# Kernel optimization log

Hardware: AMD Instinct MI355X
Metric: run time of the kernel (lower is better)

The kernel has to match this reference:

```python
import jax, jax.numpy as jnp
import numpy as np

H = 512  # hidden_dimension
B = 32
S = 2048


def setup_inputs() -> dict:
    key = jax.random.key(0)
    k1, k2, k3, k4, k5, k6 = jax.random.split(key, 6)
    decoder_hide = jax.random.normal(k1, (B, H), dtype=jnp.float32)
    encoder_out = jax.random.normal(k2, (B, S, 2 * H), dtype=jnp.float32)
    mask = jax.random.randint(k3, (B, S), 0, 2, dtype=jnp.int32)
    bound = 1.0 / np.sqrt(3 * H)
    W_attn = jax.random.uniform(k4, (3 * H, H), minval=-bound, maxval=bound, dtype=jnp.float32)
    b_attn = jax.random.uniform(k5, (H,), minval=-bound, maxval=bound, dtype=jnp.float32)
    bound_v = 1.0 / np.sqrt(H)
    v_w = jax.random.uniform(k6, (H,), minval=-bound_v, maxval=bound_v, dtype=jnp.float32)
    return {"decoder_hide": decoder_hide, "encoder_out": encoder_out, "mask": mask,
            "W_attn": W_attn, "b_attn": b_attn, "v_w": v_w}


def reference(decoder_hide, encoder_out, mask, W_attn, b_attn, v_w):
    # Split the concat-linear: cat((h, enc)) @ W == h @ W[:H] + enc @ W[H:]
    W_h = W_attn[:H]        # [H, H]
    W_e = W_attn[H:]        # [2H, H]
    dec_proj = decoder_hide @ W_h + b_attn                 # [B, H]
    enc_proj = jnp.einsum('bse,eh->bsh', encoder_out, W_e)  # [B, S, H]
    energy = jnp.tanh(enc_proj + dec_proj[:, None, :])      # [B, S, H]
    attention = jnp.einsum('bsh,h->bs', energy, v_w)        # [B, S]
    attention = jnp.where(mask == 0, jnp.float32(-100000.0), attention)
    return jax.nn.softmax(attention, axis=1)
```

## Files before the change

### kernel.cpp

```cpp
#include <hip/hip_runtime.h>
#include <hip/hip_bf16.h>
#include <math.h>

#define Hdim 512
#define Bdim 32
#define Sdim 2048
#define Kdim 1024
#define Mtot (Bdim * Sdim)

#define BM 128
#define BK 64

typedef __attribute__((ext_vector_type(8))) short short8;
typedef __attribute__((ext_vector_type(4))) float floatx4;

__device__ __forceinline__ short f2bf(float f) {
    union { float f; unsigned u; } v; v.f = f;
    unsigned r = v.u + 0x7fffu + ((v.u >> 16) & 1u);
    return (short)(r >> 16);
}

__device__ __forceinline__ short8 cvt8(float4 a, float4 b) {
    union { short8 s; __hip_bfloat162 h[4]; } u;
    u.h[0] = __float22bfloat162_rn(make_float2(a.x, a.y));
    u.h[1] = __float22bfloat162_rn(make_float2(a.z, a.w));
    u.h[2] = __float22bfloat162_rn(make_float2(b.x, b.y));
    u.h[3] = __float22bfloat162_rn(make_float2(b.z, b.w));
    return u.s;
}

__device__ __forceinline__ float fast_tanh(float x) {
    float ax = fabsf(x);
    float e  = __expf(-2.0f * ax);
    float r  = (1.0f - e) * __builtin_amdgcn_rcpf(1.0f + e);
    return copysignf(r, x);
}

__global__ __launch_bounds__(256) void prep_kernel(
    const float* __restrict__ W_attn, const float* __restrict__ dec,
    const float* __restrict__ b_attn, short* __restrict__ Wbp,
    float* __restrict__ dec_proj)
{
    const int t = threadIdx.x;
    if (blockIdx.x < 512) {
        const float* We = W_attn + Hdim * Hdim;
        __shared__ short tile[32][33];
        const int k0 = (blockIdx.x >> 4) * 32;
        const int n0 = (blockIdx.x & 15) * 32;
        const int r = t >> 5, c = t & 31;
        #pragma unroll
        for (int rr = 0; rr < 4; ++rr)
            tile[r + rr * 8][c] = f2bf(We[(size_t)(k0 + r + rr * 8) * Hdim + n0 + c]);
        __syncthreads();
        if (t < 128) {
            const int n_loc = t >> 2;
            const int q     = t & 3;
            const int nt    = (n0 + n_loc) >> 4;
            const int lnn   = (n0 + n_loc) & 15;
            const int ks    = k0 >> 5;
            short8 v;
            #pragma unroll
            for (int r2 = 0; r2 < 8; ++r2) v[r2] = tile[q * 8 + r2][n_loc];
            ((short8*)Wbp)[((nt * 32 + ks) * 64) + q * 16 + lnn] = v;
        }
    } else {
        __shared__ float partl[2][128];
        const int bid = blockIdx.x - 512;
        const int b  = bid >> 2;
        const int cb = bid & 3;
        const int c  = cb * 128 + (t & 127);
        const int kh = t >> 7;
        float acc = 0.0f;
        const int kbeg = kh * 256, kend = kbeg + 256;
        #pragma unroll 8
        for (int k = kbeg; k < kend; ++k)
            acc = fmaf(dec[b * Hdim + k], W_attn[(size_t)k * Hdim + c], acc);
        partl[kh][t & 127] = acc;
        __syncthreads();
        if (t < 128)
            dec_proj[b * Hdim + cb * 128 + t] = partl[0][t] + partl[1][t] + b_attn[cb * 128 + t];
    }
}

__device__ __forceinline__ void kstep(
    int kt, short* __restrict__ Ab, float4 (&ra)[4],
    const float* __restrict__ Ag, const short8* __restrict__ Bp,
    int w, int abase, int pf0, int pf1, int awo0, int awo1,
    floatx4 (&acc)[8][4])
{
    const size_t ks = (size_t)(kt >> 5);
    short8 b0[4], b1[4];
    #pragma unroll
    for (int j = 0; j < 4; ++j)
        b0[j] = Bp[((size_t)(w * 4 + j) * 32 + ks) * 64];
    #pragma unroll
    for (int j = 0; j < 4; ++j)
        b1[j] = Bp[((size_t)(w * 4 + j) * 32 + ks + 1) * 64];

    *(short8*)&Ab[awo0] = cvt8(ra[0], ra[1]);
    *(short8*)&Ab[awo1] = cvt8(ra[2], ra[3]);
    __syncthreads();

    if (kt + BK < Kdim) {
        const float4* g = (const float4*)(Ag + kt + BK);
        ra[0] = g[0]; ra[1] = g[1]; ra[2] = g[2]; ra[3] = g[3];
    }

    short8 af[4];
    #pragma unroll
    for (int i2 = 0; i2 < 4; ++i2)
        af[i2] = *(const short8*)&Ab[abase + i2 * 1024 + pf0];
    #pragma unroll
    for (int i2 = 0; i2 < 4; ++i2)
        #pragma unroll
        for (int j = 0; j < 4; ++j)
            acc[i2][j] = __builtin_amdgcn_mfma_f32_16x16x32_bf16(
                             af[i2], b0[j], acc[i2][j], 0, 0, 0);
    #pragma unroll
    for (int i2 = 0; i2 < 4; ++i2)
        af[i2] = *(const short8*)&Ab[abase + (i2 + 4) * 1024 + pf0];
    #pragma unroll
    for (int i2 = 0; i2 < 4; ++i2)
        #pragma unroll
        for (int j = 0; j < 4; ++j)
            acc[i2 + 4][j] = __builtin_amdgcn_mfma_f32_16x16x32_bf16(
                                 af[i2], b0[j], acc[i2 + 4][j], 0, 0, 0);
    #pragma unroll
    for (int i2 = 0; i2 < 4; ++i2)
        af[i2] = *(const short8*)&Ab[abase + i2 * 1024 + pf1];
    #pragma unroll
    for (int i2 = 0; i2 < 4; ++i2)
        #pragma unroll
        for (int j = 0; j < 4; ++j)
            acc[i2][j] = __builtin_amdgcn_mfma_f32_16x16x32_bf16(
                             af[i2], b1[j], acc[i2][j], 0, 0, 0);
    #pragma unroll
    for (int i2 = 0; i2 < 4; ++i2)
        af[i2] = *(const short8*)&Ab[abase + (i2 + 4) * 1024 + pf1];
    #pragma unroll
    for (int i2 = 0; i2 < 4; ++i2)
        #pragma unroll
        for (int j = 0; j < 4; ++j)
            acc[i2 + 4][j] = __builtin_amdgcn_mfma_f32_16x16x32_bf16(
                                 af[i2], b1[j], acc[i2 + 4][j], 0, 0, 0);
}

__global__ __launch_bounds__(512, 2) void scores_kernel(
    const float* __restrict__ enc,
    const short* __restrict__ Wbp,
    const float* __restrict__ dec_proj,
    const float* __restrict__ v_w,
    float* __restrict__ scores)
{
    __shared__ __align__(16) short Asm[2 * BM * BK];
    __shared__ float redl[BM][9];

    const int t    = threadIdx.x;
    const int row0 = blockIdx.x * BM;
    const int b    = row0 / Sdim;

    const int w    = t >> 6;
    const int lane = t & 63;
    const int ln   = lane & 15;
    const int quad = lane >> 4;

    const int sm  = t >> 2;
    const int sqb = (t & 3) * 2;
    const float* Ag = enc + (size_t)(row0 + sm) * Kdim + sqb * 8;
    const int awo0 = sm * BK + ((sqb       ^ (sm & 7)) * 8);
    const int awo1 = sm * BK + (((sqb + 1) ^ (sm & 7)) * 8);

    const int abase = ln * BK;
    const int pf0 = (quad ^ (ln & 7)) * 8;
    const int pf1 = pf0 ^ 32;

    const short8* Bp = ((const short8*)Wbp) + lane;

    floatx4 acc[8][4];
    #pragma unroll
    for (int i = 0; i < 8; ++i)
        #pragma unroll
        for (int j = 0; j < 4; ++j)
            acc[i][j] = (floatx4)(0.0f);

    float4 ra[4];
    { const float4* g = (const float4*)Ag; ra[0] = g[0]; ra[1] = g[1]; ra[2] = g[2]; ra[3] = g[3]; }

    #pragma unroll 1
    for (int kt = 0; kt < Kdim; kt += 2 * BK) {
        kstep(kt,      Asm,           ra, Ag, Bp, w, abase, pf0, pf1, awo0, awo1, acc);
        kstep(kt + BK, Asm + BM * BK, ra, Ag, Bp, w, abase, pf0, pf1, awo0, awo1, acc);
    }

    float dpv[4], vwv[4];
    #pragma unroll
    for (int j = 0; j < 4; ++j) {
        const int col = w * 64 + j * 16 + ln;
        dpv[j] = dec_proj[b * Hdim + col];
        vwv[j] = v_w[col];
    }
    #pragma unroll
    for (int i = 0; i < 8; ++i) {
        #pragma unroll
        for (int reg = 0; reg < 4; ++reg) {
            float s = 0.0f;
            #pragma unroll
            for (int j = 0; j < 4; ++j) {
                float x = acc[i][j][reg] + dpv[j];
                s = fmaf(vwv[j], fast_tanh(x), s);
            }
            s += __shfl_xor(s, 1, 64);
            s += __shfl_xor(s, 2, 64);
            s += __shfl_xor(s, 4, 64);
            s += __shfl_xor(s, 8, 64);
            if (ln == 0)
                redl[i * 16 + quad * 4 + reg][w] = s;
        }
    }
    __syncthreads();
    if (t < BM) {
        float s = 0.0f;
        #pragma unroll
        for (int wv = 0; wv < 8; ++wv) s += redl[t][wv];
        scores[row0 + t] = s;
    }
}

__global__ __launch_bounds__(256) void softmax_kernel(
    const float* __restrict__ scores, const int* __restrict__ mask,
    float* __restrict__ out)
{
    __shared__ float sred[8];
    const int b = blockIdx.x;
    const int t = threadIdx.x;
    const int lane = t & 63;
    const int wid  = t >> 6;

    float x[8];
    float m = -1e30f;
    #pragma unroll
    for (int j = 0; j < 8; ++j) {
        int idx = b * Sdim + j * 256 + t;
        float v = scores[idx];
        if (mask[idx] == 0) v = -100000.0f;
        x[j] = v;
        m = fmaxf(m, v);
    }
    #pragma unroll
    for (int off = 32; off >= 1; off >>= 1)
        m = fmaxf(m, __shfl_xor(m, off, 64));
    if (lane == 0) sred[wid] = m;
    __syncthreads();
    m = fmaxf(fmaxf(sred[0], sred[1]), fmaxf(sred[2], sred[3]));

    float s = 0.0f;
    #pragma unroll
    for (int j = 0; j < 8; ++j) {
        float e = __expf(x[j] - m);
        x[j] = e;
        s += e;
    }
    #pragma unroll
    for (int off = 32; off >= 1; off >>= 1)
        s += __shfl_xor(s, off, 64);
    if (lane == 0) sred[4 + wid] = s;
    __syncthreads();
    s = sred[4] + sred[5] + sred[6] + sred[7];

    const float inv = 1.0f / s;
    #pragma unroll
    for (int j = 0; j < 8; ++j)
        out[b * Sdim + j * 256 + t] = x[j] * inv;
}

extern "C" void kernel_launch(void* const* d_in, const int* in_sizes, int n_in,
                              void* d_out, int out_size, void* d_ws, size_t ws_size,
                              hipStream_t stream) {
    const float* dec  = (const float*)d_in[0];
    const float* enc  = (const float*)d_in[1];
    const int*   mask = (const int*)  d_in[2];
    const float* W    = (const float*)d_in[3];
    const float* ba   = (const float*)d_in[4];
    const float* vw   = (const float*)d_in[5];
    float* out = (float*)d_out;

    float* dec_proj = (float*)d_ws;
    short* Wbp      = (short*)(dec_proj + Bdim * Hdim);
    float* scores   = (float*)(Wbp + Hdim * Kdim);

    prep_kernel<<<640, 256, 0, stream>>>(W, dec, ba, Wbp, dec_proj);
    scores_kernel<<<Mtot / BM, 512, 0, stream>>>(enc, Wbp, dec_proj, vw, scores);
    softmax_kernel<<<Bdim, 256, 0, stream>>>(scores, mask, out);
}
```

Before: 427.5 us.

## Restructure scores GEMM into persistent 64-row groups with half-K double buffering

Each block now handles four 64-row groups instead of one 128-row tile. It stages 512-wide K halves of the encoder rows into a double-buffered LDS buffer, and the global loads for the next half are issued in the middle of the current half's MFMA loop. This cuts barriers per K step and overlaps the global-to-LDS conversion with compute. The trade-off is 128KB of LDS per block, so only one block fits per CU, plus a 16-float4 register stage and fewer blocks in the grid.

```diff
diff --git a/kernel.cpp b/kernel.cpp
--- a/kernel.cpp
+++ b/kernel.cpp
@@ -8,8 +8,10 @@
 #define Kdim 1024
 #define Mtot (Bdim * Sdim)
 
-#define BM 128
-#define BK 64
+#define RGROWS 64
+#define HK 512
+#define NSTEP 8
+#define RGPB 4
 
 typedef __attribute__((ext_vector_type(8))) short short8;
 typedef __attribute__((ext_vector_type(4))) float floatx4;
@@ -82,69 +84,6 @@
     }
 }
 
-__device__ __forceinline__ void kstep(
-    int kt, short* __restrict__ Ab, float4 (&ra)[4],
-    const float* __restrict__ Ag, const short8* __restrict__ Bp,
-    int w, int abase, int pf0, int pf1, int awo0, int awo1,
-    floatx4 (&acc)[8][4])
-{
-    const size_t ks = (size_t)(kt >> 5);
-    short8 b0[4], b1[4];
-    #pragma unroll
-    for (int j = 0; j < 4; ++j)
-        b0[j] = Bp[((size_t)(w * 4 + j) * 32 + ks) * 64];
-    #pragma unroll
-    for (int j = 0; j < 4; ++j)
-        b1[j] = Bp[((size_t)(w * 4 + j) * 32 + ks + 1) * 64];
-
-    *(short8*)&Ab[awo0] = cvt8(ra[0], ra[1]);
-    *(short8*)&Ab[awo1] = cvt8(ra[2], ra[3]);
-    __syncthreads();
-
-    if (kt + BK < Kdim) {
-        const float4* g = (const float4*)(Ag + kt + BK);
-        ra[0] = g[0]; ra[1] = g[1]; ra[2] = g[2]; ra[3] = g[3];
-    }
-
-    short8 af[4];
-    #pragma unroll
-    for (int i2 = 0; i2 < 4; ++i2)
-        af[i2] = *(const short8*)&Ab[abase + i2 * 1024 + pf0];
-    #pragma unroll
-    for (int i2 = 0; i2 < 4; ++i2)
-        #pragma unroll
-        for (int j = 0; j < 4; ++j)
-            acc[i2][j] = __builtin_amdgcn_mfma_f32_16x16x32_bf16(
-                             af[i2], b0[j], acc[i2][j], 0, 0, 0);
-    #pragma unroll
-    for (int i2 = 0; i2 < 4; ++i2)
-        af[i2] = *(const short8*)&Ab[abase + (i2 + 4) * 1024 + pf0];
-    #pragma unroll
-    for (int i2 = 0; i2 < 4; ++i2)
-        #pragma unroll
-        for (int j = 0; j < 4; ++j)
-            acc[i2 + 4][j] = __builtin_amdgcn_mfma_f32_16x16x32_bf16(
-                                 af[i2], b0[j], acc[i2 + 4][j], 0, 0, 0);
-    #pragma unroll
-    for (int i2 = 0; i2 < 4; ++i2)
-        af[i2] = *(const short8*)&Ab[abase + i2 * 1024 + pf1];
-    #pragma unroll
-    for (int i2 = 0; i2 < 4; ++i2)
-        #pragma unroll
-        for (int j = 0; j < 4; ++j)
-            acc[i2][j] = __builtin_amdgcn_mfma_f32_16x16x32_bf16(
-                             af[i2], b1[j], acc[i2][j], 0, 0, 0);
-    #pragma unroll
-    for (int i2 = 0; i2 < 4; ++i2)
-        af[i2] = *(const short8*)&Ab[abase + (i2 + 4) * 1024 + pf1];
-    #pragma unroll
-    for (int i2 = 0; i2 < 4; ++i2)
-        #pragma unroll
-        for (int j = 0; j < 4; ++j)
-            acc[i2 + 4][j] = __builtin_amdgcn_mfma_f32_16x16x32_bf16(
-                                 af[i2], b1[j], acc[i2 + 4][j], 0, 0, 0);
-}
-
 __global__ __launch_bounds__(512, 2) void scores_kernel(
     const float* __restrict__ enc,
     const short* __restrict__ Wbp,
@@ -152,45 +91,22 @@
     const float* __restrict__ v_w,
     float* __restrict__ scores)
 {
-    __shared__ __align__(16) short Asm[2 * BM * BK];
-    __shared__ float redl[BM][9];
+    __shared__ __align__(16) short Abuf[2][RGROWS * HK];
+    __shared__ float redl[RGROWS][9];
 
     const int t    = threadIdx.x;
-    const int row0 = blockIdx.x * BM;
-    const int b    = row0 / Sdim;
-
     const int w    = t >> 6;
     const int lane = t & 63;
     const int ln   = lane & 15;
     const int quad = lane >> 4;
 
-    const int sm  = t >> 2;
-    const int sqb = (t & 3) * 2;
-    const float* Ag = enc + (size_t)(row0 + sm) * Kdim + sqb * 8;
-    const int awo0 = sm * BK + ((sqb       ^ (sm & 7)) * 8);
-    const int awo1 = sm * BK + (((sqb + 1) ^ (sm & 7)) * 8);
-
-    const int abase = ln * BK;
+    const int b = blockIdx.x >> 3;
+    const float* Ablk = enc + (size_t)blockIdx.x * (RGPB * RGROWS) * Kdim;
+
     const int pf0 = (quad ^ (ln & 7)) * 8;
     const int pf1 = pf0 ^ 32;
 
     const short8* Bp = ((const short8*)Wbp) + lane;
-
-    floatx4 acc[8][4];
-    #pragma unroll
-    for (int i = 0; i < 8; ++i)
-        #pragma unroll
-        for (int j = 0; j < 4; ++j)
-            acc[i][j] = (floatx4)(0.0f);
-
-    float4 ra[4];
-    { const float4* g = (const float4*)Ag; ra[0] = g[0]; ra[1] = g[1]; ra[2] = g[2]; ra[3] = g[3]; }
-
-    #pragma unroll 1
-    for (int kt = 0; kt < Kdim; kt += 2 * BK) {
-        kstep(kt,      Asm,           ra, Ag, Bp, w, abase, pf0, pf1, awo0, awo1, acc);
-        kstep(kt + BK, Asm + BM * BK, ra, Ag, Bp, w, abase, pf0, pf1, awo0, awo1, acc);
-    }
 
     float dpv[4], vwv[4];
     #pragma unroll
@@ -199,31 +115,119 @@
         dpv[j] = dec_proj[b * Hdim + col];
         vwv[j] = v_w[col];
     }
-    #pragma unroll
-    for (int i = 0; i < 8; ++i) {
+
+    floatx4 acc[4][4];
+    #pragma unroll
+    for (int i = 0; i < 4; ++i)
         #pragma unroll
-        for (int reg = 0; reg < 4; ++reg) {
-            float s = 0.0f;
-            #pragma unroll
-            for (int j = 0; j < 4; ++j) {
-                float x = acc[i][j][reg] + dpv[j];
-                s = fmaf(vwv[j], fast_tanh(x), s);
+        for (int j = 0; j < 4; ++j)
+            acc[i][j] = (floatx4)(0.0f);
+
+    float4 stage[16];
+
+    #define ISSUE(hh) do {                                                    \
+        const float* p_ = Ablk + (size_t)((hh) >> 1) * RGROWS * Kdim          \
+                         + ((hh) & 1) * HK + lane * 8;                        \
+        _Pragma("unroll")                                                     \
+        for (int j_ = 0; j_ < 8; ++j_) {                                      \
+            const float4* g_ = (const float4*)(p_ + (size_t)(j_ * 8 + w) * Kdim); \
+            stage[2 * j_]     = g_[0];                                        \
+            stage[2 * j_ + 1] = g_[1];                                        \
+        }                                                                     \
+    } while (0)
+
+    #define WRITEHALF(bi_) do {                                               \
+        _Pragma("unroll")                                                     \
+        for (int j_ = 0; j_ < 8; ++j_) {                                      \
+            const int r_ = j_ * 8 + w;                                        \
+            *(short8*)&Abuf[bi_][r_ * HK + ((lane ^ (r_ & 7)) << 3)] =        \
+                cvt8(stage[2 * j_], stage[2 * j_ + 1]);                       \
+        }                                                                     \
+    } while (0)
+
+    ISSUE(0);
+    WRITEHALF(0);
+    __syncthreads();
+
+    #pragma unroll 1
+    for (int h = 0; h < 2 * RGPB; ++h) {
+        const int bi  = h & 1;
+        const short* Ab = Abuf[bi];
+        const int ksb = (h & 1) * 16;
+
+        #pragma unroll
+        for (int s = 0; s < NSTEP; ++s) {
+            const int ks = ksb + 2 * s;
+            short8 b0[4], b1[4];
+            #pragma unroll
+            for (int j = 0; j < 4; ++j)
+                b0[j] = Bp[((size_t)(w * 4 + j) * 32 + ks) * 64];
+            #pragma unroll
+            for (int j = 0; j < 4; ++j)
+                b1[j] = Bp[((size_t)(w * 4 + j) * 32 + ks + 1) * 64];
+
+            if (s == 3 && h < 2 * RGPB - 1) ISSUE(h + 1);
+
+            short8 af[4];
+            #pragma unroll
+            for (int i2 = 0; i2 < 4; ++i2)
+                af[i2] = *(const short8*)&Ab[(i2 * 16 + ln) * HK + s * 64 + pf0];
+            #pragma unroll
+            for (int i2 = 0; i2 < 4; ++i2)
+                #pragma unroll
+                for (int j = 0; j < 4; ++j)
+                    acc[i2][j] = __builtin_amdgcn_mfma_f32_16x16x32_bf16(
+                                     af[i2], b0[j], acc[i2][j], 0, 0, 0);
+            #pragma unroll
+            for (int i2 = 0; i2 < 4; ++i2)
+                af[i2] = *(const short8*)&Ab[(i2 * 16 + ln) * HK + s * 64 + pf1];
+            #pragma unroll
+            for (int i2 = 0; i2 < 4; ++i2)
+                #pragma unroll
+                for (int j = 0; j < 4; ++j)
+                    acc[i2][j] = __builtin_amdgcn_mfma_f32_16x16x32_bf16(
+                                     af[i2], b1[j], acc[i2][j], 0, 0, 0);
+        }
+
+        if (h & 1) {
+            const int rg = h >> 1;
+            #pragma unroll
+            for (int i2 = 0; i2 < 4; ++i2) {
+                #pragma unroll
+                for (int reg = 0; reg < 4; ++reg) {
+                    float s2 = 0.0f;
+                    #pragma unroll
+                    for (int j = 0; j < 4; ++j) {
+                        float x = acc[i2][j][reg] + dpv[j];
+                        s2 = fmaf(vwv[j], fast_tanh(x), s2);
+                    }
+                    s2 += __shfl_xor(s2, 1, 64);
+                    s2 += __shfl_xor(s2, 2, 64);
+                    s2 += __shfl_xor(s2, 4, 64);
+                    s2 += __shfl_xor(s2, 8, 64);
+                    if (ln == 0)
+                        redl[i2 * 16 + quad * 4 + reg][w] = s2;
+                }
             }
-            s += __shfl_xor(s, 1, 64);
-            s += __shfl_xor(s, 2, 64);
-            s += __shfl_xor(s, 4, 64);
-            s += __shfl_xor(s, 8, 64);
-            if (ln == 0)
-                redl[i * 16 + quad * 4 + reg][w] = s;
+            __syncthreads();
+            if (t < RGROWS) {
+                float s2 = 0.0f;
+                #pragma unroll
+                for (int wv = 0; wv < 8; ++wv) s2 += redl[t][wv];
+                scores[blockIdx.x * (RGPB * RGROWS) + rg * RGROWS + t] = s2;
+            }
+            #pragma unroll
+            for (int i = 0; i < 4; ++i)
+                #pragma unroll
+                for (int j = 0; j < 4; ++j)
+                    acc[i][j] = (floatx4)(0.0f);
         }
-    }
-    __syncthreads();
-    if (t < BM) {
-        float s = 0.0f;
-        #pragma unroll
-        for (int wv = 0; wv < 8; ++wv) s += redl[t][wv];
-        scores[row0 + t] = s;
-    }
+
+        if (h < 2 * RGPB - 1) WRITEHALF(bi ^ 1);
+        __syncthreads();
+    }
+    #undef ISSUE
+    #undef WRITEHALF
 }
 
 __global__ __launch_bounds__(256) void softmax_kernel(
@@ -289,6 +293,6 @@
     float* scores   = (float*)(Wbp + Hdim * Kdim);
 
     prep_kernel<<<640, 256, 0, stream>>>(W, dec, ba, Wbp, dec_proj);
-    scores_kernel<<<Mtot / BM, 512, 0, stream>>>(enc, Wbp, dec_proj, vw, scores);
+    scores_kernel<<<Mtot / (RGPB * RGROWS), 512, 0, stream>>>(enc, Wbp, dec_proj, vw, scores);
     softmax_kernel<<<Bdim, 256, 0, stream>>>(scores, mask, out);
 }
```

New measurement: 438.6 us. 1.03x slower.
